# Kernel tuning notes

Hardware: AMD Instinct MI355X
Metric: run time of the kernel (lower is better)

The kernel has to match this reference:

```python
import jax, jax.numpy as jnp
import numpy as np

POOLED_H = 7
POOLED_W = 7
SPATIAL_SCALE = 0.0625
B, C, H, W = 8, 256, 48, 48
R = 300
IMG = 768  # = H / SPATIAL_SCALE


def setup_inputs() -> dict:
    key = jax.random.key(0)
    k1, k2, k3, k4 = jax.random.split(key, 4)
    features = jax.random.normal(k1, (B, C, H, W), dtype=jnp.float32)
    # rois: (batch_idx, x1, y1, x2, y2) in input-image coords
    bidx = jax.random.randint(k2, (R, 1), 0, B).astype(jnp.float32)
    tl = jax.random.uniform(k3, (R, 2), minval=0.0, maxval=IMG - 64.0)
    wh = jax.random.uniform(k4, (R, 2), minval=32.0, maxval=320.0)
    br = jnp.minimum(tl + wh, IMG - 1.0)
    rois = jnp.concatenate([bidx, tl, br], axis=1).astype(jnp.float32)
    return {"features": features, "rois": rois}


def _hat_integral(x, grid):
    """Integral from -inf to x of the unit hat basis function centered at each
    grid point g (support [g-1, g+1], peak 1, total mass 1).
    x: [..., 1-broadcastable], grid: [G] -> returns [..., G]."""
    t = x[..., None] - (grid - 1.0)
    return jnp.where(
        t <= 0.0, 0.0,
        jnp.where(t <= 1.0, 0.5 * t * t,
                  jnp.where(t <= 2.0, 1.0 - 0.5 * (2.0 - t) ** 2, 1.0)))


def reference(features, rois):
    # Precise RoI Pooling: exact double integral of the bilinear interpolant
    # over each bin, divided by bin area. Bilinear interp (with zero padding
    # outside the map, as in the CUDA PrRoIPoolingGetData) is
    #   f(u,v) = sum_{j,i} feat[j,i] * hat_j(v) * hat_i(u)
    # so the bin integral factorizes into per-axis hat-integral weights.
    Bf, Cf, Hf, Wf = features.shape
    bidx = rois[:, 0].astype(jnp.int32)
    x1 = rois[:, 1] * SPATIAL_SCALE
    y1 = rois[:, 2] * SPATIAL_SCALE
    x2 = rois[:, 3] * SPATIAL_SCALE
    y2 = rois[:, 4] * SPATIAL_SCALE
    roi_w = jnp.maximum(x2 - x1, 0.0)
    roi_h = jnp.maximum(y2 - y1, 0.0)
    bin_w = roi_w / POOLED_W  # [R]
    bin_h = roi_h / POOLED_H

    ph = jnp.arange(POOLED_H, dtype=jnp.float32)
    pw = jnp.arange(POOLED_W, dtype=jnp.float32)
    ya = y1[:, None] + ph[None, :] * bin_h[:, None]  # [R, PH]
    yb = ya + bin_h[:, None]
    xa = x1[:, None] + pw[None, :] * bin_w[:, None]  # [R, PW]
    xb = xa + bin_w[:, None]

    gy = jnp.arange(Hf, dtype=jnp.float32)
    gx = jnp.arange(Wf, dtype=jnp.float32)
    Wy = _hat_integral(yb, gy) - _hat_integral(ya, gy)  # [R, PH, H]
    Wx = _hat_integral(xb, gx) - _hat_integral(xa, gx)  # [R, PW, W]

    feat = features[bidx]  # [R, C, H, W]
    t = jnp.einsum('rpj,rcji->rcpi', Wy, feat)   # integrate over y
    num = jnp.einsum('rqi,rcpi->rcpq', Wx, t)    # integrate over x -> [R,C,PH,PW]

    area = (bin_w * bin_h)[:, None, None, None]  # win_size per ROI
    out = jnp.where(area > 0.0, num / jnp.where(area > 0.0, area, 1.0), 0.0)
    return out
```

## Files before the change

kernel.cpp:

```cpp
#include <hip/hip_runtime.h>


#define PH 7
#define PW 7
#define NBINS 49
#define SCALE 0.0625f
#define CH 256
#define FH 48
#define FW 48
#define RNUM 300
#define CB 8
#define MAXJ 23
#define ROWF 28
#define PRM 128

__device__ __forceinline__ float hat_int(float x, float g) {
    float t = x - (g - 1.0f);
    if (t <= 0.0f) return 0.0f;
    if (t <= 1.0f) return 0.5f * t * t;
    if (t <= 2.0f) { float u = 2.0f - t; return 1.0f - 0.5f * u * u; }
    return 1.0f;
}

__global__ __launch_bounds__(256)
void prroi_prep(const float* __restrict__ rois, float* __restrict__ prm) {
    const int r = blockIdx.x * 4 + (threadIdx.x >> 6);
    const int t = threadIdx.x & 63;
    if (r >= RNUM || t >= 15) return;

    const float* roi = rois + r * 5;
    const int   b  = (int)roi[0];
    const float x1 = roi[1] * SCALE, y1 = roi[2] * SCALE;
    const float x2 = roi[3] * SCALE, y2 = roi[4] * SCALE;
    const float roi_w = fmaxf(x2 - x1, 0.0f), roi_h = fmaxf(y2 - y1, 0.0f);
    const float bin_w = roi_w / (float)PW, bin_h = roi_h / (float)PH;
    const float area = bin_w * bin_h;
    const float inv_area = (area > 0.0f) ? (1.0f / area) : 0.0f;

    const float ylo = fminf(y1, y2), yhi = fmaxf(y1, y2);
    const float xlo = fminf(x1, x2), xhi = fmaxf(x1, x2);
    const int j1 = min(FH - 1, (int)floorf(yhi) + 1);
    const int i1 = min(FW - 1, (int)floorf(xhi) + 1);
    const int J0 = min(max(0, (int)floorf(ylo) - 1), FH - 6);
    const int I0 = min(max(0, (int)floorf(xlo) - 1) & ~3, FW - 8);
    const int JROWS = min(FH - J0, max(j1 - J0 + 1, 6));
    int NI4 = min(((i1 - I0) >> 2) + 1, (FW - I0) >> 2);
    NI4 = max(NI4, 2);

    float* p = prm + (size_t)r * PRM;
    if (t < PH) {
        const int ph = t;
        const float ya = y1 + ph * bin_h, yb = ya + bin_h;
        const int base = min(max((int)floorf(ya) - 1, J0), J0 + JROWS - 6);
#pragma unroll
        for (int k = 0; k < 6; ++k) {
            const float g = (float)(base + k);
            p[ph * 8 + k] = (hat_int(yb, g) - hat_int(ya, g)) * inv_area;
        }
        p[ph * 8 + 6] = __int_as_float(base - J0);
        p[ph * 8 + 7] = 0.0f;
    } else if (t < PH + PW) {
        const int pw = t - PH;
        const float xa = x1 + pw * bin_w, xb = xa + bin_w;
        const int base = min(max((int)floorf(xa) - 1, I0), I0 + 4 * NI4 - 6);
#pragma unroll
        for (int k = 0; k < 6; ++k) {
            const float g = (float)(base + k);
            p[56 + pw * 8 + k] = hat_int(xb, g) - hat_int(xa, g);
        }
        p[56 + pw * 8 + 6] = __int_as_float(base - I0);
        p[56 + pw * 8 + 7] = 0.0f;
    } else {
        p[112] = __int_as_float(b);
        p[113] = __int_as_float(J0);
        p[114] = __int_as_float(I0);
        p[115] = __int_as_float(JROWS | (NI4 << 8));
    }
}

__global__ __launch_bounds__(256)
void prroi_main(const float* __restrict__ feat,
                const float* __restrict__ prm,
                float* __restrict__ out) {
    const int cblk = blockIdx.x;
    const int r    = blockIdx.y;
    const int c0   = cblk * CB;
    const int tid  = threadIdx.x;

    __shared__ float patch[MAXJ * ROWF * CB];
    __shared__ float rs[PW * MAXJ * CB];

    const float* p = prm + (size_t)r * PRM;

    const float4 misc = *(const float4*)(p + 112);
    const int qA  = tid & 1;
    const int pwA = (tid >> 1) & 7;
    const int jA  = tid >> 4;
    const float4 wxv0 = *(const float4*)(p + 56 + pwA * 8);
    const float4 wxv1 = *(const float4*)(p + 56 + pwA * 8 + 4);
    const int bin = tid & 63;
    const int cp  = tid >> 6;
    const int phv = bin / 7;
    const int pwv = bin - phv * 7;
    const float4 wyv0 = *(const float4*)(p + phv * 8);
    const float4 wyv1 = *(const float4*)(p + phv * 8 + 4);

    const int b      = __float_as_int(misc.x);
    const int J0     = __float_as_int(misc.y);
    const int I0     = __float_as_int(misc.z);
    const int packed = __float_as_int(misc.w);
    const int JROWS  = packed & 255;
    const int NI4    = packed >> 8;
    const int biA    = __float_as_int(wxv1.z);
    const int bj     = __float_as_int(wyv1.z);

    const int i4P = tid & 7;
    const int qP  = (tid >> 3) & 1;
    const int jbP = tid >> 4;
    if (i4P < NI4) {
        const float* src = feat + (size_t)(b * CH + c0 + 4 * qP) * FH * FW
                         + (size_t)(J0 + jbP) * FW + I0 + 4 * i4P;
        float* dst = &patch[((size_t)jbP * ROWF + 4 * i4P) * CB + 4 * qP];
        for (int j = jbP; j < JROWS; j += 16) {
            const float4 v0 = *(const float4*)(src);
            const float4 v1 = *(const float4*)(src + FH * FW);
            const float4 v2 = *(const float4*)(src + 2 * FH * FW);
            const float4 v3 = *(const float4*)(src + 3 * FH * FW);
            *(float4*)(dst + 0 * CB) = make_float4(v0.x, v1.x, v2.x, v3.x);
            *(float4*)(dst + 1 * CB) = make_float4(v0.y, v1.y, v2.y, v3.y);
            *(float4*)(dst + 2 * CB) = make_float4(v0.z, v1.z, v2.z, v3.z);
            *(float4*)(dst + 3 * CB) = make_float4(v0.w, v1.w, v2.w, v3.w);
            src += 16 * FW;
            dst += 16 * ROWF * CB;
        }
    }
    __syncthreads();

    if (pwA < PW) {
        const float* base0 = &patch[((size_t)jA * ROWF + biA) * CB + 4 * qA];
        float* rdst = &rs[((size_t)pwA * MAXJ + jA) * CB + 4 * qA];
        for (int j = jA; j < JROWS; j += 16) {
            float ax, ay, az, aw;
            {
                const float4 v = *(const float4*)(base0 + 0 * CB);
                ax = wxv0.x * v.x; ay = wxv0.x * v.y; az = wxv0.x * v.z; aw = wxv0.x * v.w;
            }
            {
                const float4 v = *(const float4*)(base0 + 1 * CB);
                ax += wxv0.y * v.x; ay += wxv0.y * v.y; az += wxv0.y * v.z; aw += wxv0.y * v.w;
            }
            {
                const float4 v = *(const float4*)(base0 + 2 * CB);
                ax += wxv0.z * v.x; ay += wxv0.z * v.y; az += wxv0.z * v.z; aw += wxv0.z * v.w;
            }
            {
                const float4 v = *(const float4*)(base0 + 3 * CB);
                ax += wxv0.w * v.x; ay += wxv0.w * v.y; az += wxv0.w * v.z; aw += wxv0.w * v.w;
            }
            {
                const float4 v = *(const float4*)(base0 + 4 * CB);
                ax += wxv1.x * v.x; ay += wxv1.x * v.y; az += wxv1.x * v.z; aw += wxv1.x * v.w;
            }
            {
                const float4 v = *(const float4*)(base0 + 5 * CB);
                ax += wxv1.y * v.x; ay += wxv1.y * v.y; az += wxv1.y * v.z; aw += wxv1.y * v.w;
            }
            *(float4*)rdst = make_float4(ax, ay, az, aw);
            base0 += 16 * ROWF * CB;
            rdst  += 16 * CB;
        }
    }
    __syncthreads();

    if (bin < NBINS) {
        const float* rbase = &rs[((size_t)pwv * MAXJ + bj) * CB + 2 * cp];
        float ax = 0.0f, ay = 0.0f;
        {
            const float2 v = *(const float2*)(rbase + 0 * CB);
            ax += wyv0.x * v.x; ay += wyv0.x * v.y;
        }
        {
            const float2 v = *(const float2*)(rbase + 1 * CB);
            ax += wyv0.y * v.x; ay += wyv0.y * v.y;
        }
        {
            const float2 v = *(const float2*)(rbase + 2 * CB);
            ax += wyv0.z * v.x; ay += wyv0.z * v.y;
        }
        {
            const float2 v = *(const float2*)(rbase + 3 * CB);
            ax += wyv0.w * v.x; ay += wyv0.w * v.y;
        }
        {
            const float2 v = *(const float2*)(rbase + 4 * CB);
            ax += wyv1.x * v.x; ay += wyv1.x * v.y;
        }
        {
            const float2 v = *(const float2*)(rbase + 5 * CB);
            ax += wyv1.y * v.x; ay += wyv1.y * v.y;
        }
        float* o = out + ((size_t)r * CH + c0 + 2 * cp) * NBINS + bin;
        o[0]     = ax;
        o[NBINS] = ay;
    }
}

extern "C" void kernel_launch(void* const* d_in, const int* in_sizes, int n_in,
                              void* d_out, int out_size, void* d_ws, size_t ws_size,
                              hipStream_t stream) {
    const float* feat = (const float*)d_in[0];
    const float* rois = (const float*)d_in[1];
    float* out = (float*)d_out;
    float* prm = (float*)d_ws;

    prroi_prep<<<(RNUM + 3) / 4, 256, 0, stream>>>(rois, prm);
    prroi_main<<<dim3(CH / CB, RNUM), 256, 0, stream>>>(feat, prm, out);
}
```

Baseline: 89.28 us.

## Process two ROIs per block and prefetch second ROI patch during first

Each block now handles two consecutive ROIs for the same channel group, halving the grid. The first global load batch for the second ROI's patch is issued before the first ROI's x-pass, and the data is written into shared memory after the first ROI's y-pass, so the load latency overlaps compute. The cost is more registers for the second ROI's weights and prefetch buffers, half as many blocks for latency hiding, and an extra sync sequence per block.

```diff
diff --git a/kernel.cpp b/kernel.cpp
--- a/kernel.cpp
+++ b/kernel.cpp
@@ -78,50 +78,119 @@
     }
 }
 
+__device__ __forceinline__ void do_PA(const float* __restrict__ patch,
+                                      float* __restrict__ rs,
+                                      int jA, int qA, int pwA, int biA, int JROWS,
+                                      const float4& wxv0, const float4& wxv1) {
+    if (pwA < PW) {
+        const float* base0 = &patch[((size_t)jA * ROWF + biA) * CB + 4 * qA];
+        float* rdst = &rs[((size_t)pwA * MAXJ + jA) * CB + 4 * qA];
+        for (int j = jA; j < JROWS; j += 16) {
+            float ax, ay, az, aw;
+            {
+                const float4 v = *(const float4*)(base0 + 0 * CB);
+                ax = wxv0.x * v.x; ay = wxv0.x * v.y; az = wxv0.x * v.z; aw = wxv0.x * v.w;
+            }
+            {
+                const float4 v = *(const float4*)(base0 + 1 * CB);
+                ax += wxv0.y * v.x; ay += wxv0.y * v.y; az += wxv0.y * v.z; aw += wxv0.y * v.w;
+            }
+            {
+                const float4 v = *(const float4*)(base0 + 2 * CB);
+                ax += wxv0.z * v.x; ay += wxv0.z * v.y; az += wxv0.z * v.z; aw += wxv0.z * v.w;
+            }
+            {
+                const float4 v = *(const float4*)(base0 + 3 * CB);
+                ax += wxv0.w * v.x; ay += wxv0.w * v.y; az += wxv0.w * v.z; aw += wxv0.w * v.w;
+            }
+            {
+                const float4 v = *(const float4*)(base0 + 4 * CB);
+                ax += wxv1.x * v.x; ay += wxv1.x * v.y; az += wxv1.x * v.z; aw += wxv1.x * v.w;
+            }
+            {
+                const float4 v = *(const float4*)(base0 + 5 * CB);
+                ax += wxv1.y * v.x; ay += wxv1.y * v.y; az += wxv1.y * v.z; aw += wxv1.y * v.w;
+            }
+            *(float4*)rdst = make_float4(ax, ay, az, aw);
+            base0 += (size_t)16 * ROWF * CB;
+            rdst  += 16 * CB;
+        }
+    }
+}
+
+__device__ __forceinline__ void do_PB(const float* __restrict__ rs,
+                                      float* __restrict__ out,
+                                      int r, int c0, int bin, int cp, int pwv, int bj,
+                                      const float4& wyv0, const float4& wyv1) {
+    if (bin < NBINS) {
+        const float* rbase = &rs[((size_t)pwv * MAXJ + bj) * CB + 2 * cp];
+        float ax = 0.0f, ay = 0.0f;
+        { const float2 v = *(const float2*)(rbase + 0 * CB); ax += wyv0.x * v.x; ay += wyv0.x * v.y; }
+        { const float2 v = *(const float2*)(rbase + 1 * CB); ax += wyv0.y * v.x; ay += wyv0.y * v.y; }
+        { const float2 v = *(const float2*)(rbase + 2 * CB); ax += wyv0.z * v.x; ay += wyv0.z * v.y; }
+        { const float2 v = *(const float2*)(rbase + 3 * CB); ax += wyv0.w * v.x; ay += wyv0.w * v.y; }
+        { const float2 v = *(const float2*)(rbase + 4 * CB); ax += wyv1.x * v.x; ay += wyv1.x * v.y; }
+        { const float2 v = *(const float2*)(rbase + 5 * CB); ax += wyv1.y * v.x; ay += wyv1.y * v.y; }
+        float* o = out + ((size_t)r * CH + c0 + 2 * cp) * NBINS + bin;
+        o[0]     = ax;
+        o[NBINS] = ay;
+    }
+}
+
 __global__ __launch_bounds__(256)
 void prroi_main(const float* __restrict__ feat,
                 const float* __restrict__ prm,
                 float* __restrict__ out) {
     const int cblk = blockIdx.x;
-    const int r    = blockIdx.y;
+    const int r0   = 2 * blockIdx.y;
+    const int r1   = r0 + 1;
     const int c0   = cblk * CB;
     const int tid  = threadIdx.x;
 
     __shared__ float patch[MAXJ * ROWF * CB];
     __shared__ float rs[PW * MAXJ * CB];
 
-    const float* p = prm + (size_t)r * PRM;
-
-    const float4 misc = *(const float4*)(p + 112);
+    const float* p0 = prm + (size_t)r0 * PRM;
+    const float* p1 = prm + (size_t)r1 * PRM;
+
+    const float4 misc0 = *(const float4*)(p0 + 112);
+    const float4 misc1 = *(const float4*)(p1 + 112);
     const int qA  = tid & 1;
     const int pwA = (tid >> 1) & 7;
     const int jA  = tid >> 4;
-    const float4 wxv0 = *(const float4*)(p + 56 + pwA * 8);
-    const float4 wxv1 = *(const float4*)(p + 56 + pwA * 8 + 4);
+    const float4 wx0v0 = *(const float4*)(p0 + 56 + pwA * 8);
+    const float4 wx0v1 = *(const float4*)(p0 + 56 + pwA * 8 + 4);
+    const float4 wx1v0 = *(const float4*)(p1 + 56 + pwA * 8);
+    const float4 wx1v1 = *(const float4*)(p1 + 56 + pwA * 8 + 4);
     const int bin = tid & 63;
     const int cp  = tid >> 6;
     const int phv = bin / 7;
     const int pwv = bin - phv * 7;
-    const float4 wyv0 = *(const float4*)(p + phv * 8);
-    const float4 wyv1 = *(const float4*)(p + phv * 8 + 4);
-
-    const int b      = __float_as_int(misc.x);
-    const int J0     = __float_as_int(misc.y);
-    const int I0     = __float_as_int(misc.z);
-    const int packed = __float_as_int(misc.w);
-    const int JROWS  = packed & 255;
-    const int NI4    = packed >> 8;
-    const int biA    = __float_as_int(wxv1.z);
-    const int bj     = __float_as_int(wyv1.z);
+    const float4 wy0v0 = *(const float4*)(p0 + phv * 8);
+    const float4 wy0v1 = *(const float4*)(p0 + phv * 8 + 4);
+    const float4 wy1v0 = *(const float4*)(p1 + phv * 8);
+    const float4 wy1v1 = *(const float4*)(p1 + phv * 8 + 4);
+
+    const int b0 = __float_as_int(misc0.x), J00 = __float_as_int(misc0.y);
+    const int I00 = __float_as_int(misc0.z);
+    const int pk0 = __float_as_int(misc0.w);
+    const int JROWS0 = pk0 & 255, NI40 = pk0 >> 8;
+    const int b1 = __float_as_int(misc1.x), J01 = __float_as_int(misc1.y);
+    const int I01 = __float_as_int(misc1.z);
+    const int pk1 = __float_as_int(misc1.w);
+    const int JROWS1 = pk1 & 255, NI41 = pk1 >> 8;
+    const int biA0 = __float_as_int(wx0v1.z), bj0 = __float_as_int(wy0v1.z);
+    const int biA1 = __float_as_int(wx1v1.z), bj1 = __float_as_int(wy1v1.z);
 
     const int i4P = tid & 7;
     const int qP  = (tid >> 3) & 1;
     const int jbP = tid >> 4;
-    if (i4P < NI4) {
-        const float* src = feat + (size_t)(b * CH + c0 + 4 * qP) * FH * FW
-                         + (size_t)(J0 + jbP) * FW + I0 + 4 * i4P;
+
+    if (i4P < NI40) {
+        const float* src = feat + (size_t)(b0 * CH + c0 + 4 * qP) * FH * FW
+                         + (size_t)(J00 + jbP) * FW + I00 + 4 * i4P;
         float* dst = &patch[((size_t)jbP * ROWF + 4 * i4P) * CB + 4 * qP];
-        for (int j = jbP; j < JROWS; j += 16) {
+        for (int j = jbP; j < JROWS0; j += 16) {
             const float4 v0 = *(const float4*)(src);
             const float4 v1 = *(const float4*)(src + FH * FW);
             const float4 v2 = *(const float4*)(src + 2 * FH * FW);
@@ -131,78 +200,50 @@
             *(float4*)(dst + 2 * CB) = make_float4(v0.z, v1.z, v2.z, v3.z);
             *(float4*)(dst + 3 * CB) = make_float4(v0.w, v1.w, v2.w, v3.w);
             src += 16 * FW;
-            dst += 16 * ROWF * CB;
-        }
-    }
-    __syncthreads();
-
-    if (pwA < PW) {
-        const float* base0 = &patch[((size_t)jA * ROWF + biA) * CB + 4 * qA];
-        float* rdst = &rs[((size_t)pwA * MAXJ + jA) * CB + 4 * qA];
-        for (int j = jA; j < JROWS; j += 16) {
-            float ax, ay, az, aw;
-            {
-                const float4 v = *(const float4*)(base0 + 0 * CB);
-                ax = wxv0.x * v.x; ay = wxv0.x * v.y; az = wxv0.x * v.z; aw = wxv0.x * v.w;
-            }
-            {
-                const float4 v = *(const float4*)(base0 + 1 * CB);
-                ax += wxv0.y * v.x; ay += wxv0.y * v.y; az += wxv0.y * v.z; aw += wxv0.y * v.w;
-            }
-            {
-                const float4 v = *(const float4*)(base0 + 2 * CB);
-                ax += wxv0.z * v.x; ay += wxv0.z * v.y; az += wxv0.z * v.z; aw += wxv0.z * v.w;
-            }
-            {
-                const float4 v = *(const float4*)(base0 + 3 * CB);
-                ax += wxv0.w * v.x; ay += wxv0.w * v.y; az += wxv0.w * v.z; aw += wxv0.w * v.w;
-            }
-            {
-                const float4 v = *(const float4*)(base0 + 4 * CB);
-                ax += wxv1.x * v.x; ay += wxv1.x * v.y; az += wxv1.x * v.z; aw += wxv1.x * v.w;
-            }
-            {
-                const float4 v = *(const float4*)(base0 + 5 * CB);
-                ax += wxv1.y * v.x; ay += wxv1.y * v.y; az += wxv1.y * v.z; aw += wxv1.y * v.w;
-            }
-            *(float4*)rdst = make_float4(ax, ay, az, aw);
-            base0 += 16 * ROWF * CB;
-            rdst  += 16 * CB;
-        }
-    }
-    __syncthreads();
-
-    if (bin < NBINS) {
-        const float* rbase = &rs[((size_t)pwv * MAXJ + bj) * CB + 2 * cp];
-        float ax = 0.0f, ay = 0.0f;
-        {
-            const float2 v = *(const float2*)(rbase + 0 * CB);
-            ax += wyv0.x * v.x; ay += wyv0.x * v.y;
-        }
-        {
-            const float2 v = *(const float2*)(rbase + 1 * CB);
-            ax += wyv0.y * v.x; ay += wyv0.y * v.y;
-        }
-        {
-            const float2 v = *(const float2*)(rbase + 2 * CB);
-            ax += wyv0.z * v.x; ay += wyv0.z * v.y;
-        }
-        {
-            const float2 v = *(const float2*)(rbase + 3 * CB);
-            ax += wyv0.w * v.x; ay += wyv0.w * v.y;
-        }
-        {
-            const float2 v = *(const float2*)(rbase + 4 * CB);
-            ax += wyv1.x * v.x; ay += wyv1.x * v.y;
-        }
-        {
-            const float2 v = *(const float2*)(rbase + 5 * CB);
-            ax += wyv1.y * v.x; ay += wyv1.y * v.y;
-        }
-        float* o = out + ((size_t)r * CH + c0 + 2 * cp) * NBINS + bin;
-        o[0]     = ax;
-        o[NBINS] = ay;
-    }
+            dst += (size_t)16 * ROWF * CB;
+        }
+    }
+    float4 u0, u1, u2, u3;
+    const bool have1 = (i4P < NI41) && (jbP < JROWS1);
+    const float* src1 = feat + (size_t)(b1 * CH + c0 + 4 * qP) * FH * FW
+                      + (size_t)(J01 + jbP) * FW + I01 + 4 * i4P;
+    if (have1) {
+        u0 = *(const float4*)(src1);
+        u1 = *(const float4*)(src1 + FH * FW);
+        u2 = *(const float4*)(src1 + 2 * FH * FW);
+        u3 = *(const float4*)(src1 + 3 * FH * FW);
+    }
+    __syncthreads();
+
+    do_PA(patch, rs, jA, qA, pwA, biA0, JROWS0, wx0v0, wx0v1);
+    __syncthreads();
+
+    do_PB(rs, out, r0, c0, bin, cp, pwv, bj0, wy0v0, wy0v1);
+    if (have1) {
+        float* dst = &patch[((size_t)jbP * ROWF + 4 * i4P) * CB + 4 * qP];
+        *(float4*)(dst + 0 * CB) = make_float4(u0.x, u1.x, u2.x, u3.x);
+        *(float4*)(dst + 1 * CB) = make_float4(u0.y, u1.y, u2.y, u3.y);
+        *(float4*)(dst + 2 * CB) = make_float4(u0.z, u1.z, u2.z, u3.z);
+        *(float4*)(dst + 3 * CB) = make_float4(u0.w, u1.w, u2.w, u3.w);
+        if (jbP + 16 < JROWS1) {
+            const float* s2 = src1 + 16 * FW;
+            const float4 w0 = *(const float4*)(s2);
+            const float4 w1 = *(const float4*)(s2 + FH * FW);
+            const float4 w2 = *(const float4*)(s2 + 2 * FH * FW);
+            const float4 w3 = *(const float4*)(s2 + 3 * FH * FW);
+            float* d2 = dst + (size_t)16 * ROWF * CB;
+            *(float4*)(d2 + 0 * CB) = make_float4(w0.x, w1.x, w2.x, w3.x);
+            *(float4*)(d2 + 1 * CB) = make_float4(w0.y, w1.y, w2.y, w3.y);
+            *(float4*)(d2 + 2 * CB) = make_float4(w0.z, w1.z, w2.z, w3.z);
+            *(float4*)(d2 + 3 * CB) = make_float4(w0.w, w1.w, w2.w, w3.w);
+        }
+    }
+    __syncthreads();
+
+    do_PA(patch, rs, jA, qA, pwA, biA1, JROWS1, wx1v0, wx1v1);
+    __syncthreads();
+
+    do_PB(rs, out, r1, c0, bin, cp, pwv, bj1, wy1v0, wy1v1);
 }
 
 extern "C" void kernel_launch(void* const* d_in, const int* in_sizes, int n_in,
@@ -214,5 +255,5 @@
     float* prm = (float*)d_ws;
 
     prroi_prep<<<(RNUM + 3) / 4, 256, 0, stream>>>(rois, prm);
-    prroi_main<<<dim3(CH / CB, RNUM), 256, 0, stream>>>(feat, prm, out);
-}
+    prroi_main<<<dim3(CH / CB, RNUM / 2), 256, 0, stream>>>(feat, prm, out);
+}
```

Result: slower. 92.02 us (+3.1%).
